# Optimization experiments

Measured on AMD Instinct MI355X. Metric: run time of the kernel, lower is better.

The kernel has to match this reference:

```python
import jax, jax.numpy as jnp
import numpy as np
import math

SEQ_LEN, PRED_LEN, CHANNELS, RANK = 720, 336, 862, 32
IN_LEN = SEQ_LEN // 2  # Haar low-pass with stride 2 (seq_len even)
BATCH = 256


def _dct2_ortho_mat(N):
    # D[k, n] = s_k * 2 * cos(pi * k * (2n+1) / (2N)); orthonormal DCT-II
    k = np.arange(N)[:, None]
    n = np.arange(N)[None, :]
    D = 2.0 * np.cos(np.pi * k * (2 * n + 1) / (2 * N))
    s = np.full(N, np.sqrt(1.0 / (2 * N)))
    s[0] = np.sqrt(1.0 / (4 * N))
    return jnp.asarray((s[:, None] * D).astype(np.float32))


def _idct2_unnorm_mat(N):
    # scipy.fft.idct(type=2, norm=None): out[n] = (1/N) * (x0/2 + sum_{k>=1} x_k cos(pi k (2n+1)/(2N)))
    # Returned as M[k, n] so that out = x @ M along last axis.
    k = np.arange(N)[:, None]
    n = np.arange(N)[None, :]
    M = np.cos(np.pi * k * (2 * n + 1) / (2 * N)) / N
    M[0, :] *= 0.5
    return jnp.asarray(M.astype(np.float32))


D_DCT = _dct2_ortho_mat(IN_LEN)        # [IN_LEN, IN_LEN]
M_IDCT = _idct2_unnorm_mat(PRED_LEN)   # [PRED_LEN, PRED_LEN]
INV_SQRT2 = 1.0 / math.sqrt(2.0)


def setup_inputs() -> dict:
    key = jax.random.key(0)
    k1, k2, k3, k4 = jax.random.split(key, 4)
    x = jax.random.normal(k1, (BATCH, SEQ_LEN, CHANNELS), dtype=jnp.float32)
    # kaiming_uniform-like scales for LowRank params
    boundA = math.sqrt(6.0 / IN_LEN)
    boundB = math.sqrt(6.0 / RANK)
    A = jax.random.uniform(k2, (IN_LEN, RANK), dtype=jnp.float32, minval=-boundA, maxval=boundA)
    B = jax.random.uniform(k3, (RANK, PRED_LEN), dtype=jnp.float32, minval=-boundB, maxval=boundB)
    b = jax.random.uniform(k4, (PRED_LEN,), dtype=jnp.float32)
    return {"x": x, "A": A, "B": B, "b": b}


def reference(x, A, B, b):
    # x: [B, L, C] -> [B, C, L]
    xt = jnp.transpose(x, (0, 2, 1))
    seq_mean = jnp.mean(xt, axis=-1, keepdims=True)          # [B, C, 1]
    xc = xt - seq_mean
    # Haar low-pass: depthwise conv1d with [1,1]/sqrt(2), stride 2
    h = (xc[..., ::2] + xc[..., 1::2]) * INV_SQRT2           # [B, C, IN_LEN]
    # orthonormal DCT-II along last axis, then divide by length
    y = jnp.einsum('bcn,kn->bck', h, D_DCT) / IN_LEN         # [B, C, IN_LEN]
    # low-rank prediction head (shared across channels)
    z = (y @ A) @ B + b                                      # [B, C, PRED_LEN]
    # unnormalized inverse DCT-II (scipy idct type=2, norm=None)
    o = z @ M_IDCT                                           # [B, C, PRED_LEN]
    o = o + seq_mean
    return jnp.transpose(o, (0, 2, 1))                       # [B, PRED_LEN, C]
```

## Files before the change

kernel.cpp:

```cpp
#include <hip/hip_runtime.h>
#include <math.h>

#define SEQ_LEN   720
#define IN_LEN    360
#define PRED_LEN  336
#define CHANNELS  862
#define RANK      32
#define BATCH     256

typedef _Float16 h2 __attribute__((ext_vector_type(2)));

#define WS_WP    0
#define WS_VT    11520
#define WS_CVEC  22272
#define WS_WH    22608
#define WS_VH    28368

__device__ __forceinline__ float fdot2w(h2 a, h2 b, float c) {
#if __has_builtin(__builtin_amdgcn_fdot2)
    return __builtin_amdgcn_fdot2(a, b, c, false);
#else
    return fmaf((float)a[0], (float)b[0], fmaf((float)a[1], (float)b[1], c));
#endif
}
__device__ __forceinline__ h2 pkrtz(float a, float b) {
    return __builtin_bit_cast(h2, __builtin_amdgcn_cvt_pkrtz(a, b));
}
#define BC(u) __builtin_bit_cast(h2, (u))

__global__ __launch_bounds__(256) void k_prep(const float* __restrict__ A,
                                              const float* __restrict__ B,
                                              const float* __restrict__ bias,
                                              float* __restrict__ Wp,
                                              float* __restrict__ Vt,
                                              float* __restrict__ cvec) {
    __shared__ float sbuf[IN_LEN * RANK];
    int blk = blockIdx.x;
    if (blk < 45) {
        for (int i = threadIdx.x; i < IN_LEN * RANK; i += 256) sbuf[i] = A[i];
        __syncthreads();
        int idx = blk * 256 + threadIdx.x;
        int n = idx >> 5, r = idx & 31;
        int step = 2 * n + 1, m = 0;
        float sum = 0.f;
        for (int k = 0; k < IN_LEN; ++k) {
            float coef = (k == 0) ? 0.05270462766947299f
                                  : 0.07453559924999299f;
            float d = coef * cospif((float)m * (1.0f / 720.0f));
            sum = fmaf(d, sbuf[k * RANK + r], sum);
            m += step; if (m >= 1440) m -= 1440;
        }
        Wp[idx] = sum * 0.0019641855032960957f;
    } else if (blk < 87) {
        for (int i = threadIdx.x; i < PRED_LEN * RANK; i += 256) {
            int r = i / PRED_LEN, k = i - r * PRED_LEN;
            sbuf[k * RANK + r] = B[i];
        }
        __syncthreads();
        int idx = (blk - 45) * 256 + threadIdx.x;
        int n = idx >> 5, r = idx & 31;
        int step = 2 * n + 1, m = 0;
        float sum = 0.f;
        for (int k = 0; k < PRED_LEN; ++k) {
            float mk = cospif((float)m * (1.0f / 672.0f));
            if (k == 0) mk *= 0.5f;
            sum = fmaf(mk, sbuf[k * RANK + r], sum);
            m += step; if (m >= 1344) m -= 1344;
        }
        Vt[idx] = sum * (1.0f / 336.0f);
    } else {
        int n = (blk - 87) * 256 + threadIdx.x;
        if (n < PRED_LEN) {
            int step = 2 * n + 1, m = 0;
            float sum = 0.f;
            for (int k = 0; k < PRED_LEN; ++k) {
                float mk = cospif((float)m * (1.0f / 672.0f));
                if (k == 0) mk *= 0.5f;
                sum = fmaf(mk, bias[k], sum);
                m += step; if (m >= 1344) m -= 1344;
            }
            cvec[n] = sum * (1.0f / 336.0f);
        }
    }
}

__global__ __launch_bounds__(256) void k_pack(const float* __restrict__ Wp,
                                              const float* __restrict__ Vt,
                                              unsigned* __restrict__ Wh,
                                              unsigned* __restrict__ Vh) {
    int idx = blockIdx.x * 256 + threadIdx.x;
    if (idx < 5760) {
        int np = idx >> 5, r = idx & 31;
        h2 v = pkrtz(Wp[(2 * np) * RANK + r], Wp[(2 * np + 1) * RANK + r]);
        Wh[idx] = __builtin_bit_cast(unsigned, v);
    } else if (idx < 5760 + 5376) {
        int j = idx - 5760;
        int n = j >> 4, q = j & 15;
        h2 v = pkrtz(Vt[n * RANK + 2 * q], Vt[n * RANK + 2 * q + 1]);
        Vh[j] = __builtin_bit_cast(unsigned, v);
    }
}

__global__ __launch_bounds__(256) void k_main(const float* __restrict__ x,
                                              const float* __restrict__ A,
                                              const unsigned* __restrict__ Wh,
                                              const unsigned* __restrict__ Vh,
                                              const float* __restrict__ cvec,
                                              float* __restrict__ out) {
    __shared__ uint4 lds4[1440];
    unsigned* ldsu = (unsigned*)lds4;
    const int tid = threadIdx.x;
    const int b = blockIdx.y;
    const int c0 = 2 * (blockIdx.x * 256 + tid);
    const bool active = (c0 < CHANNELS);

    {
        const uint4* s = (const uint4*)Wh;
        for (int i = tid; i < 1440; i += 256) lds4[i] = s[i];
    }
    __syncthreads();

    float acc0[RANK], acc1[RANK];
    #pragma unroll
    for (int r = 0; r < RANK; ++r) { acc0[r] = 0.f; acc1[r] = 0.f; }
    float S0 = 0.f, S1 = 0.f, mean0 = 0.f, mean1 = 0.f;
    h2 th0[16], th1[16];

    if (active) {
        const float* xp = x + (size_t)b * (SEQ_LEN * CHANNELS) + c0;

        float2 bufA[8], bufB[8];
        #define LOADB(BUF, BD) { const float* p_ = xp + (size_t)(BD) * (8 * CHANNELS); \
            _Pragma("unroll") \
            for (int j_ = 0; j_ < 8; ++j_) BUF[j_] = *(const float2*)(p_ + j_ * CHANNELS); }

        #define NPBODY(BUF, S) { \
            float pe0 = BUF[4*S+0].x + BUF[4*S+1].x; \
            float pe1 = BUF[4*S+0].y + BUF[4*S+1].y; \
            float po0 = BUF[4*S+2].x + BUF[4*S+3].x; \
            float po1 = BUF[4*S+2].y + BUF[4*S+3].y; \
            S0 += pe0 + po0; S1 += pe1 + po1; \
            h2 P0 = pkrtz(pe0, po0); \
            h2 P1 = pkrtz(pe1, po1); \
            _Pragma("unroll") \
            for (int q_ = 0; q_ < 8; ++q_) { \
                uint4 wv = wr[8*S + q_]; \
                acc0[4*q_+0] = fdot2w(P0, BC(wv.x), acc0[4*q_+0]); \
                acc1[4*q_+0] = fdot2w(P1, BC(wv.x), acc1[4*q_+0]); \
                acc0[4*q_+1] = fdot2w(P0, BC(wv.y), acc0[4*q_+1]); \
                acc1[4*q_+1] = fdot2w(P1, BC(wv.y), acc1[4*q_+1]); \
                acc0[4*q_+2] = fdot2w(P0, BC(wv.z), acc0[4*q_+2]); \
                acc1[4*q_+2] = fdot2w(P1, BC(wv.z), acc1[4*q_+2]); \
                acc0[4*q_+3] = fdot2w(P0, BC(wv.w), acc0[4*q_+3]); \
                acc1[4*q_+3] = fdot2w(P1, BC(wv.w), acc1[4*q_+3]); \
            } }

        #define BODY(BUF, BD) { const uint4* wr = lds4 + 16 * (BD); \
            NPBODY(BUF, 0); NPBODY(BUF, 1); }

        LOADB(bufA, 0)
        for (int it = 0; it < 45; ++it) {
            LOADB(bufB, 2 * it + 1)
            BODY(bufA, 2 * it)
            if (it < 44) LOADB(bufA, 2 * it + 2)
            BODY(bufB, 2 * it + 1)
        }
        #undef BODY
        #undef NPBODY
        #undef LOADB

        const float k360 = (1.0f / 360.0f) * 0.037267799624996496f;
        float g0 = -S0 * k360, g1 = -S1 * k360;
        #pragma unroll
        for (int q = 0; q < 8; ++q) {
            float4 a4 = ((const float4*)A)[q];
            acc0[4*q+0] = fmaf(g0, a4.x, acc0[4*q+0]);
            acc1[4*q+0] = fmaf(g1, a4.x, acc1[4*q+0]);
            acc0[4*q+1] = fmaf(g0, a4.y, acc0[4*q+1]);
            acc1[4*q+1] = fmaf(g1, a4.y, acc1[4*q+1]);
            acc0[4*q+2] = fmaf(g0, a4.z, acc0[4*q+2]);
            acc1[4*q+2] = fmaf(g1, a4.z, acc1[4*q+2]);
            acc0[4*q+3] = fmaf(g0, a4.w, acc0[4*q+3]);
            acc1[4*q+3] = fmaf(g1, a4.w, acc1[4*q+3]);
        }
        mean0 = S0 * (1.0f / 720.0f);
        mean1 = S1 * (1.0f / 720.0f);

        #pragma unroll
        for (int u = 0; u < 16; ++u) {
            th0[u] = pkrtz(acc0[2*u], acc0[2*u+1]);
            th1[u] = pkrtz(acc1[2*u], acc1[2*u+1]);
        }
    }
    __syncthreads();

    {
        const uint4* s = (const uint4*)Vh;
        for (int i = tid; i < 1344; i += 256) lds4[i] = s[i];
        for (int i = tid; i < PRED_LEN; i += 256)
            ldsu[5376 + i] = __float_as_uint(cvec[i]);
    }
    __syncthreads();

    if (active) {
        float* op = out + (size_t)b * (PRED_LEN * CHANNELS) + c0;
        #pragma unroll 2
        for (int n = 0; n < PRED_LEN; ++n) {
            const uint4* vr = lds4 + n * 4;
            float oA0 = 0.f, oB0 = 0.f, oA1 = 0.f, oB1 = 0.f;
            #pragma unroll
            for (int q = 0; q < 4; ++q) {
                uint4 v = vr[q];
                oA0 = fdot2w(th0[4*q+0], BC(v.x), oA0);
                oA1 = fdot2w(th1[4*q+0], BC(v.x), oA1);
                oB0 = fdot2w(th0[4*q+1], BC(v.y), oB0);
                oB1 = fdot2w(th1[4*q+1], BC(v.y), oB1);
                oA0 = fdot2w(th0[4*q+2], BC(v.z), oA0);
                oA1 = fdot2w(th1[4*q+2], BC(v.z), oA1);
                oB0 = fdot2w(th0[4*q+3], BC(v.w), oB0);
                oB1 = fdot2w(th1[4*q+3], BC(v.w), oB1);
            }
            float cvn = __uint_as_float(ldsu[5376 + n]);
            float2 o;
            o.x = (oA0 + oB0) + cvn + mean0;
            o.y = (oA1 + oB1) + cvn + mean1;
            *(float2*)op = o;
            op += CHANNELS;
        }
    }
}


extern "C" void kernel_launch(void* const* d_in, const int* in_sizes, int n_in,
                              void* d_out, int out_size, void* d_ws, size_t ws_size,
                              hipStream_t stream) {
    (void)in_sizes; (void)n_in; (void)out_size; (void)ws_size;
    const float* x    = (const float*)d_in[0];
    const float* A    = (const float*)d_in[1];
    const float* B    = (const float*)d_in[2];
    const float* bias = (const float*)d_in[3];
    float* out = (float*)d_out;
    float* ws  = (float*)d_ws;

    float*    Wp   = ws + WS_WP;
    float*    Vt   = ws + WS_VT;
    float*    cvec = ws + WS_CVEC;
    unsigned* Wh   = (unsigned*)(ws + WS_WH);
    unsigned* Vh   = (unsigned*)(ws + WS_VH);

    k_prep<<<dim3(89), dim3(256), 0, stream>>>(A, B, bias, Wp, Vt, cvec);
    k_pack<<<dim3(44), dim3(256), 0, stream>>>(Wp, Vt, Wh, Vh);
    k_main<<<dim3(2, BATCH), dim3(256), 0, stream>>>(x, A, Wh, Vh, cvec, out);
}
```

Baseline: 298.8 us.

## Use one 448-thread block per batch and preload both weight tables into LDS

```diff
diff --git a/kernel.cpp b/kernel.cpp
--- a/kernel.cpp
+++ b/kernel.cpp
@@ -101,23 +101,22 @@
     }
 }
 
-__global__ __launch_bounds__(256) void k_main(const float* __restrict__ x,
+__global__ __launch_bounds__(448) void k_main(const float* __restrict__ x,
                                               const float* __restrict__ A,
                                               const unsigned* __restrict__ Wh,
                                               const unsigned* __restrict__ Vh,
                                               const float* __restrict__ cvec,
                                               float* __restrict__ out) {
-    __shared__ uint4 lds4[1440];
+    __shared__ uint4 lds4[2868];
     unsigned* ldsu = (unsigned*)lds4;
     const int tid = threadIdx.x;
-    const int b = blockIdx.y;
-    const int c0 = 2 * (blockIdx.x * 256 + tid);
-    const bool active = (c0 < CHANNELS);
-
-    {
-        const uint4* s = (const uint4*)Wh;
-        for (int i = tid; i < 1440; i += 256) lds4[i] = s[i];
-    }
+    const int b = blockIdx.x;
+    const int c0 = 2 * tid;
+    const bool active = (tid < 431);
+
+    for (int i = tid; i < 1440; i += 448) lds4[i] = ((const uint4*)Wh)[i];
+    for (int i = tid; i < 1344; i += 448) lds4[1440 + i] = ((const uint4*)Vh)[i];
+    for (int i = tid; i < PRED_LEN; i += 448) ldsu[11136 + i] = __float_as_uint(cvec[i]);
     __syncthreads();
 
     float acc0[RANK], acc1[RANK];
@@ -134,17 +133,17 @@
             _Pragma("unroll") \
             for (int j_ = 0; j_ < 8; ++j_) BUF[j_] = *(const float2*)(p_ + j_ * CHANNELS); }
 
-        #define NPBODY(BUF, S) { \
-            float pe0 = BUF[4*S+0].x + BUF[4*S+1].x; \
-            float pe1 = BUF[4*S+0].y + BUF[4*S+1].y; \
-            float po0 = BUF[4*S+2].x + BUF[4*S+3].x; \
-            float po1 = BUF[4*S+2].y + BUF[4*S+3].y; \
+        #define NPBODY(BUF, S_) { \
+            float pe0 = BUF[4*S_+0].x + BUF[4*S_+1].x; \
+            float pe1 = BUF[4*S_+0].y + BUF[4*S_+1].y; \
+            float po0 = BUF[4*S_+2].x + BUF[4*S_+3].x; \
+            float po1 = BUF[4*S_+2].y + BUF[4*S_+3].y; \
             S0 += pe0 + po0; S1 += pe1 + po1; \
             h2 P0 = pkrtz(pe0, po0); \
             h2 P1 = pkrtz(pe1, po1); \
             _Pragma("unroll") \
             for (int q_ = 0; q_ < 8; ++q_) { \
-                uint4 wv = wr[8*S + q_]; \
+                uint4 wv = wr[8*S_ + q_]; \
                 acc0[4*q_+0] = fdot2w(P0, BC(wv.x), acc0[4*q_+0]); \
                 acc1[4*q_+0] = fdot2w(P1, BC(wv.x), acc1[4*q_+0]); \
                 acc0[4*q_+1] = fdot2w(P0, BC(wv.y), acc0[4*q_+1]); \
@@ -191,22 +190,11 @@
             th0[u] = pkrtz(acc0[2*u], acc0[2*u+1]);
             th1[u] = pkrtz(acc1[2*u], acc1[2*u+1]);
         }
-    }
-    __syncthreads();
-
-    {
-        const uint4* s = (const uint4*)Vh;
-        for (int i = tid; i < 1344; i += 256) lds4[i] = s[i];
-        for (int i = tid; i < PRED_LEN; i += 256)
-            ldsu[5376 + i] = __float_as_uint(cvec[i]);
-    }
-    __syncthreads();
-
-    if (active) {
+
         float* op = out + (size_t)b * (PRED_LEN * CHANNELS) + c0;
         #pragma unroll 2
         for (int n = 0; n < PRED_LEN; ++n) {
-            const uint4* vr = lds4 + n * 4;
+            const uint4* vr = lds4 + 1440 + n * 4;
             float oA0 = 0.f, oB0 = 0.f, oA1 = 0.f, oB1 = 0.f;
             #pragma unroll
             for (int q = 0; q < 4; ++q) {
@@ -220,7 +208,7 @@
                 oB0 = fdot2w(th0[4*q+3], BC(v.w), oB0);
                 oB1 = fdot2w(th1[4*q+3], BC(v.w), oB1);
             }
-            float cvn = __uint_as_float(ldsu[5376 + n]);
+            float cvn = __uint_as_float(ldsu[11136 + n]);
             float2 o;
             o.x = (oA0 + oB0) + cvn + mean0;
             o.y = (oA1 + oB1) + cvn + mean1;
@@ -250,5 +238,5 @@
 
     k_prep<<<dim3(89), dim3(256), 0, stream>>>(A, B, bias, Wp, Vt, cvec);
     k_pack<<<dim3(44), dim3(256), 0, stream>>>(Wp, Vt, Wh, Vh);
-    k_main<<<dim3(2, BATCH), dim3(256), 0, stream>>>(x, A, Wh, Vh, cvec, out);
-}
+    k_main<<<dim3(BATCH), dim3(448), 0, stream>>>(x, A, Wh, Vh, cvec, out);
+}
```

After: 290.2 us. 2.9% less time.
